# Kernel tuning notes

Measured on AMD Instinct MI355X. Metric: run time of the kernel, lower is better.

## Reference

```python
import jax, jax.numpy as jnp
import numpy as np

VOCAB, EMBED = 100000, 128
B, QLEN, DLEN = 1024, 32, 256
KERNEL_NUM, SIGMA, EXACT_SIGMA = 11, 0.1, 0.001
EPS = 1e-8  # torch F.cosine_similarity eps


def _kernel_mus(n):
    l_mu = [1.0]
    if n == 1:
        return l_mu
    bin_size = 2.0 / (n - 1)
    l_mu.append(1 - bin_size / 2)
    for i in range(1, n - 1):
        l_mu.append(round(l_mu[i] - bin_size, 5))
    return list(reversed(l_mu))


def _kernel_sigmas(n, sigma, exact_sigma):
    l_sigma = [exact_sigma]
    if n == 1:
        return l_sigma
    l_sigma += [sigma] * (n - 1)
    return list(reversed(l_sigma))


MUS = jnp.asarray(np.array(_kernel_mus(KERNEL_NUM), dtype=np.float32))      # [K]
SIGMAS = jnp.asarray(np.array(_kernel_sigmas(KERNEL_NUM, SIGMA, EXACT_SIGMA), dtype=np.float32))  # [K]


def setup_inputs() -> dict:
    key = jax.random.key(0)
    k = jax.random.split(key, 7)
    return {
        "emb": jax.random.normal(k[0], (VOCAB, EMBED), dtype=jnp.float32),
        "mlp_w": jax.random.normal(k[1], (1, KERNEL_NUM), dtype=jnp.float32) * 0.3,
        "mlp_b": jax.random.normal(k[2], (1,), dtype=jnp.float32) * 0.1,
        "query1": jax.random.randint(k[3], (B, QLEN), 0, VOCAB, dtype=jnp.int32).astype(jnp.int64),
        "doc1": jax.random.randint(k[4], (B, DLEN), 0, VOCAB, dtype=jnp.int32).astype(jnp.int64),
        "query2": jax.random.randint(k[5], (B, QLEN), 0, VOCAB, dtype=jnp.int32).astype(jnp.int64),
        "doc2": jax.random.randint(k[6], (B, DLEN), 0, VOCAB, dtype=jnp.int32).astype(jnp.int64),
    }


def _predict(emb, mlp_w, mlp_b, query, doc):
    qe = emb[query]                               # [B,Q,E]
    de = emb[doc]                                 # [B,D,E]
    qn = jnp.linalg.norm(qe, axis=-1)             # [B,Q]
    dn = jnp.linalg.norm(de, axis=-1)             # [B,D]
    dots = jnp.einsum("bqe,bde->bqd", qe, de)    # [B,Q,D]
    sim = dots / jnp.maximum(qn[:, :, None] * dn[:, None, :], EPS)
    # multi-Gaussian soft histogram: exp(-(sim-mu)^2/(2 sigma^2)), sum over doc,
    # log1p, sum over query  -> [B,K]
    z = (sim[..., None] - MUS) / SIGMAS           # [B,Q,D,K]
    K = jnp.exp(-0.5 * z * z)
    pooled = jnp.log1p(K.sum(axis=2)).sum(axis=1)  # [B,K]
    return pooled @ mlp_w.T + mlp_b               # [B,1]


def reference(emb, mlp_w, mlp_b, query1, doc1, query2, doc2):
    logits_1 = _predict(emb, mlp_w, mlp_b, query1, doc1)
    logits_2 = _predict(emb, mlp_w, mlp_b, query2, doc2)
    return jax.nn.sigmoid(logits_1 - logits_2)    # [B,1]
```

## Files before the change

kernel.cpp:

```cpp
#include <hip/hip_runtime.h>
#include <math.h>

#define VOCAB 100000
#define NB    1024
#define QLEN  32
#define DLEN  256
#define EMBED 128
#define KNUM  11

typedef __attribute__((ext_vector_type(8))) short bf16x8;
typedef __attribute__((ext_vector_type(4))) float f32x4;

#define HALF_L2E 0.7213475204444817f
#define TWO_L2E  2.8853900817779268f
#define EM4      0.018315638888734179f

#define SSTR  68
#define SHALF (16 * SSTR)

__global__ __launch_bounds__(256)
void cvt_table(const float* __restrict__ emb, ushort* __restrict__ ebf,
               float* __restrict__ inorm)
{
    const int row = blockIdx.x * 8 + (threadIdx.x >> 5);
    const int l32 = threadIdx.x & 31;
    const float4 v = *((const float4*)(emb + (size_t)row * EMBED) + l32);
    union { float f; unsigned u; } x0, x1, x2, x3;
    x0.f = v.x; x1.f = v.y; x2.f = v.z; x3.f = v.w;
    const unsigned r0 = x0.u + 0x8000u, r1 = x1.u + 0x8000u;
    const unsigned r2 = x2.u + 0x8000u, r3 = x3.u + 0x8000u;
    uint2 packed;
    packed.x = (r0 >> 16) | (r1 & 0xFFFF0000u);
    packed.y = (r2 >> 16) | (r3 & 0xFFFF0000u);
    *((uint2*)(ebf + (size_t)row * EMBED) + l32) = packed;
    x0.u = r0 & 0xFFFF0000u; x1.u = r1 & 0xFFFF0000u;
    x2.u = r2 & 0xFFFF0000u; x3.u = r3 & 0xFFFF0000u;
    float n = x0.f * x0.f + x1.f * x1.f + x2.f * x2.f + x3.f * x3.f;
    #pragma unroll
    for (int m = 1; m < 32; m <<= 1) n += __shfl_xor(n, m);
    if (l32 == 0) inorm[row] = __builtin_amdgcn_rsqf(n);
}

__device__ __forceinline__ bf16x8 cvt8(const float* p, float& nacc)
{
    uint4 a = *((const uint4*)p);
    uint4 b = *((const uint4*)(p + 4));
    unsigned u[8] = {a.x, a.y, a.z, a.w, b.x, b.y, b.z, b.w};
    bf16x8 r;
    #pragma unroll
    for (int i = 0; i < 8; ++i) {
        const unsigned q = u[i] + 0x8000u;
        r[i] = (short)(q >> 16);
        union { unsigned uu; float ff; } g; g.uu = q & 0xFFFF0000u;
        nacc = fmaf(g.ff, g.ff, nacc);
    }
    return r;
}

__device__ __forceinline__ void pool_half(float* __restrict__ wtile,
                                          const f32x4* __restrict__ a,
                                          const float* __restrict__ riq,
                                          const float* __restrict__ idn,
                                          float (*__restrict__ stot)[12],
                                          int mtbase, int l15, int quad)
{
    #pragma unroll
    for (int nt = 0; nt < 4; ++nt)
        #pragma unroll
        for (int r = 0; r < 4; ++r)
            wtile[(quad * 4 + r) * SSTR + nt * 16 + l15] = a[nt][r] * riq[r] * idn[nt];

    const float* rp = wtile + l15 * SSTR + quad * 16;
    float ksum[KNUM];
    #pragma unroll
    for (int k = 0; k < KNUM; ++k) ksum[k] = 0.f;

    #pragma unroll
    for (int i = 0; i < 4; ++i) {
        const f32x4 sv = *((const f32x4*)(rp + 4 * i));
        #pragma unroll
        for (int e = 0; e < 4; ++e) {
            const float s  = sv[e];
            const float z  = fmaf(s, 10.f, -1.f);
            const float e0 = exp2f(-HALF_L2E * (z * z));
            float ru = exp2f(fmaf(z,  TWO_L2E, -TWO_L2E));
            float rd = exp2f(fmaf(z, -TWO_L2E, -TWO_L2E));
            ksum[5] += e0;
            float tt = e0;
            tt *= ru; ksum[6] += tt; ru *= EM4;
            tt *= ru; ksum[7] += tt; ru *= EM4;
            tt *= ru; ksum[8] += tt; ru *= EM4;
            tt *= ru; ksum[9] += tt;
            tt = e0;
            tt *= rd; ksum[4] += tt; rd *= EM4;
            tt *= rd; ksum[3] += tt; rd *= EM4;
            tt *= rd; ksum[2] += tt; rd *= EM4;
            tt *= rd; ksum[1] += tt; rd *= EM4;
            tt *= rd; ksum[0] += tt;
            ksum[10] += (s > 0.995f) ? 1.f : 0.f;
        }
    }
    #pragma unroll
    for (int k = 0; k < KNUM; ++k) {
        ksum[k] += __shfl_xor(ksum[k], 16);
        ksum[k] += __shfl_xor(ksum[k], 32);
    }
    if (quad == 0) {
        #pragma unroll
        for (int k = 0; k < KNUM; ++k)
            atomicAdd(&stot[mtbase + l15][k], ksum[k]);
    }
}

template<bool PRE>
__global__ __launch_bounds__(256, 2)
void knrm_fused(const float* __restrict__ emb,
                const ushort* __restrict__ ebf,
                const float* __restrict__ inorm,
                const float* __restrict__ mlp_w,
                const int* __restrict__ q1, const int* __restrict__ d1,
                const int* __restrict__ q2, const int* __restrict__ d2,
                float* __restrict__ out)
{
    const int b    = blockIdx.x;
    const int t    = threadIdx.x;
    const int w    = t >> 6;
    const int l15  = t & 15;
    const int quad = (t & 63) >> 4;

    const int* __restrict__ qryA = q1 + b * QLEN;
    const int* __restrict__ docA = d1 + b * DLEN;
    const int* __restrict__ qryB = q2 + b * QLEN;
    const int* __restrict__ docB = d2 + b * DLEN;

    __shared__ __align__(16) float s_sim[4 * SHALF];
    __shared__ float s_tot[2][QLEN][12];

    #pragma unroll
    for (int i = t; i < 2 * QLEN * 12; i += 256) ((float*)s_tot)[i] = 0.f;
    __syncthreads();

    const int qidA0 = qryA[l15], qidA1 = qryA[l15 + 16];
    const int qidB0 = qryB[l15], qidB1 = qryB[l15 + 16];
    int didA[4], didB[4];
    #pragma unroll
    for (int nt = 0; nt < 4; ++nt) {
        didA[nt] = docA[(w * 4 + nt) * 16 + l15];
        didB[nt] = docB[(w * 4 + nt) * 16 + l15];
    }

    f32x4 acc[2][4];
    #pragma unroll
    for (int mt = 0; mt < 2; ++mt)
        #pragma unroll
        for (int nt = 0; nt < 4; ++nt)
            acc[mt][nt] = (f32x4){0.f, 0.f, 0.f, 0.f};

    float idnA[4], idnB[4], riqA[2][4], riqB[2][4];
    float* wtile = s_sim + w * SHALF;

    if (PRE) {
        const ushort* qa0 = ebf + (size_t)qidA0 * EMBED + quad * 8;
        const ushort* qa1 = ebf + (size_t)qidA1 * EMBED + quad * 8;
        #pragma unroll
        for (int kk = 0; kk < 4; ++kk) {
            const bf16x8 a0 = *((const bf16x8*)(qa0 + kk * 32));
            const bf16x8 a1 = *((const bf16x8*)(qa1 + kk * 32));
            #pragma unroll
            for (int nt = 0; nt < 4; ++nt) {
                const bf16x8 bb = *((const bf16x8*)(ebf + (size_t)didA[nt] * EMBED + quad * 8 + kk * 32));
                acc[0][nt] = __builtin_amdgcn_mfma_f32_16x16x32_bf16(a0, bb, acc[0][nt], 0, 0, 0);
                acc[1][nt] = __builtin_amdgcn_mfma_f32_16x16x32_bf16(a1, bb, acc[1][nt], 0, 0, 0);
            }
        }

        bf16x8 pq0[4], pq1[4], pdb[4][4];
        const ushort* qb0 = ebf + (size_t)qidB0 * EMBED + quad * 8;
        const ushort* qb1 = ebf + (size_t)qidB1 * EMBED + quad * 8;
        #pragma unroll
        for (int kk = 0; kk < 4; ++kk) {
            pq0[kk] = *((const bf16x8*)(qb0 + kk * 32));
            pq1[kk] = *((const bf16x8*)(qb1 + kk * 32));
            #pragma unroll
            for (int nt = 0; nt < 4; ++nt)
                pdb[nt][kk] = *((const bf16x8*)(ebf + (size_t)didB[nt] * EMBED + quad * 8 + kk * 32));
        }
        #pragma unroll
        for (int nt = 0; nt < 4; ++nt) { idnA[nt] = inorm[didA[nt]]; idnB[nt] = inorm[didB[nt]]; }
        #pragma unroll
        for (int r = 0; r < 4; ++r) {
            riqA[0][r] = inorm[qryA[quad * 4 + r]];
            riqA[1][r] = inorm[qryA[16 + quad * 4 + r]];
            riqB[0][r] = inorm[qryB[quad * 4 + r]];
            riqB[1][r] = inorm[qryB[16 + quad * 4 + r]];
        }

        pool_half(wtile, acc[0], riqA[0], idnA, s_tot[0], 0,  l15, quad);
        pool_half(wtile, acc[1], riqA[1], idnA, s_tot[0], 16, l15, quad);

        #pragma unroll
        for (int mt = 0; mt < 2; ++mt)
            #pragma unroll
            for (int nt = 0; nt < 4; ++nt)
                acc[mt][nt] = (f32x4){0.f, 0.f, 0.f, 0.f};
        #pragma unroll
        for (int kk = 0; kk < 4; ++kk)
            #pragma unroll
            for (int nt = 0; nt < 4; ++nt) {
                acc[0][nt] = __builtin_amdgcn_mfma_f32_16x16x32_bf16(pq0[kk], pdb[nt][kk], acc[0][nt], 0, 0, 0);
                acc[1][nt] = __builtin_amdgcn_mfma_f32_16x16x32_bf16(pq1[kk], pdb[nt][kk], acc[1][nt], 0, 0, 0);
            }

        pool_half(wtile, acc[0], riqB[0], idnB, s_tot[1], 0,  l15, quad);
        pool_half(wtile, acc[1], riqB[1], idnB, s_tot[1], 16, l15, quad);
    } else {
        #pragma unroll
        for (int p = 0; p < 2; ++p) {
            const int* qry = p == 0 ? qryA : qryB;
            const int qi0 = p == 0 ? qidA0 : qidB0;
            const int qi1 = p == 0 ? qidA1 : qidB1;
            const int* did = p == 0 ? didA : didB;
            float qn2[2] = {0.f, 0.f}, dn2[4] = {0.f, 0.f, 0.f, 0.f};
            #pragma unroll
            for (int mt = 0; mt < 2; ++mt)
                #pragma unroll
                for (int nt = 0; nt < 4; ++nt)
                    acc[mt][nt] = (f32x4){0.f, 0.f, 0.f, 0.f};
            const float* qp0 = emb + (size_t)qi0 * EMBED + quad * 8;
            const float* qp1 = emb + (size_t)qi1 * EMBED + quad * 8;
            #pragma unroll
            for (int kk = 0; kk < 4; ++kk) {
                const bf16x8 a0 = cvt8(qp0 + kk * 32, qn2[0]);
                const bf16x8 a1 = cvt8(qp1 + kk * 32, qn2[1]);
                #pragma unroll
                for (int nt = 0; nt < 4; ++nt) {
                    const bf16x8 bb = cvt8(emb + (size_t)did[nt] * EMBED + quad * 8 + kk * 32, dn2[nt]);
                    acc[0][nt] = __builtin_amdgcn_mfma_f32_16x16x32_bf16(a0, bb, acc[0][nt], 0, 0, 0);
                    acc[1][nt] = __builtin_amdgcn_mfma_f32_16x16x32_bf16(a1, bb, acc[1][nt], 0, 0, 0);
                }
            }
            float idn[4], riq[2][4];
            #pragma unroll
            for (int i = 0; i < 2; ++i) {
                qn2[i] += __shfl_xor(qn2[i], 16);
                qn2[i] += __shfl_xor(qn2[i], 32);
            }
            #pragma unroll
            for (int nt = 0; nt < 4; ++nt) {
                dn2[nt] += __shfl_xor(dn2[nt], 16);
                dn2[nt] += __shfl_xor(dn2[nt], 32);
                idn[nt] = __builtin_amdgcn_rsqf(dn2[nt]);
            }
            #pragma unroll
            for (int r = 0; r < 4; ++r) {
                riq[0][r] = __builtin_amdgcn_rsqf(__shfl(qn2[0], quad * 4 + r));
                riq[1][r] = __builtin_amdgcn_rsqf(__shfl(qn2[1], quad * 4 + r));
            }
            pool_half(wtile, acc[0], riq[0], idn, s_tot[p], 0,  l15, quad);
            pool_half(wtile, acc[1], riq[1], idn, s_tot[p], 16, l15, quad);
        }
    }
    __syncthreads();

    if (t < QLEN) {
        float c = 0.f;
        #pragma unroll
        for (int k = 0; k < KNUM; ++k)
            c += mlp_w[k] * (log1pf(s_tot[0][t][k]) - log1pf(s_tot[1][t][k]));
        #pragma unroll
        for (int mm = 1; mm < 32; mm <<= 1) c += __shfl_xor(c, mm);
        if (t == 0) out[b] = 1.f / (1.f + __expf(-c));
    }
}

extern "C" void kernel_launch(void* const* d_in, const int* in_sizes, int n_in,
                              void* d_out, int out_size, void* d_ws, size_t ws_size,
                              hipStream_t stream)
{
    const float* emb   = (const float*)d_in[0];
    const float* mlp_w = (const float*)d_in[1];
    const int* q1 = (const int*)d_in[3];
    const int* d1 = (const int*)d_in[4];
    const int* q2 = (const int*)d_in[5];
    const int* d2 = (const int*)d_in[6];

    float* out = (float*)d_out;

    const size_t need = (size_t)VOCAB * 4
                      + (size_t)VOCAB * EMBED * 2 + 256;
    if (ws_size >= need) {
        float*  inorm = (float*)d_ws;
        ushort* ebf   = (ushort*)(inorm + VOCAB);
        cvt_table<<<VOCAB / 8, 256, 0, stream>>>(emb, ebf, inorm);
        knrm_fused<true><<<NB, 256, 0, stream>>>(emb, ebf, inorm, mlp_w,
                                                 q1, d1, q2, d2, out);
    } else {
        knrm_fused<false><<<NB, 256, 0, stream>>>(emb, nullptr, nullptr, mlp_w,
                                                  q1, d1, q2, d2, out);
    }
}
```

Baseline: 145.8 us.

## Split query/doc pairs across grid and stage bf16 rows via global_load_lds

The fused kernel, which did both prediction pairs per block, is replaced by a 2D grid with one block per (batch, pair). Each block stages the gathered bf16 embedding rows straight into LDS using global_load_lds, then feeds MFMA from LDS. The goal is more parallel blocks and asynchronous direct-to-LDS gathers in place of register-held loads. The cost is a third kernel launch to combine the logits through sigmoid, plus a larger LDS footprint (about 72KB per block) that may limit occupancy.

```diff
diff --git a/kernel.cpp b/kernel.cpp
--- a/kernel.cpp
+++ b/kernel.cpp
@@ -17,6 +17,13 @@
 
 #define SSTR  68
 #define SHALF (16 * SSTR)
+
+typedef const __attribute__((address_space(1))) unsigned int gu32;
+typedef __attribute__((address_space(3))) unsigned int lu32;
+__device__ __forceinline__ void load_lds16(const void* g, void* l)
+{
+    __builtin_amdgcn_global_load_lds((gu32*)g, (lu32*)l, 16, 0, 0);
+}
 
 __global__ __launch_bounds__(256)
 void cvt_table(const float* __restrict__ emb, ushort* __restrict__ ebf,
@@ -112,15 +119,103 @@
     }
 }
 
-template<bool PRE>
+__global__ __launch_bounds__(256)
+void knrm_pair(const ushort* __restrict__ ebf,
+               const float* __restrict__ inorm,
+               const float* __restrict__ mlp_w,
+               const int* __restrict__ q1, const int* __restrict__ d1,
+               const int* __restrict__ q2, const int* __restrict__ d2,
+               float* __restrict__ logits)
+{
+    const int b    = blockIdx.x;
+    const int pair = blockIdx.y;
+    const int t    = threadIdx.x;
+    const int w    = t >> 6;
+    const int lane = t & 63;
+    const int l15  = t & 15;
+    const int quad = lane >> 4;
+
+    const int* __restrict__ qry = (pair == 0 ? q1 : q2) + b * QLEN;
+    const int* __restrict__ doc = (pair == 0 ? d1 : d2) + b * DLEN;
+
+    __shared__ __align__(16) char s_stage[4 * 16 * 1024 + 8 * 1024];
+    __shared__ float s_tot[QLEN][12];
+    char* dstage = s_stage;
+    char* qstage = s_stage + 4 * 16 * 1024;
+
+    #pragma unroll
+    for (int i = t; i < QLEN * 12; i += 256) ((float*)s_tot)[i] = 0.f;
+
+    int did[4];
+    #pragma unroll
+    for (int nt = 0; nt < 4; ++nt) did[nt] = doc[(w * 4 + nt) * 16 + l15];
+
+    #pragma unroll
+    for (int nt = 0; nt < 4; ++nt)
+        #pragma unroll
+        for (int kk = 0; kk < 4; ++kk)
+            load_lds16(ebf + (size_t)did[nt] * EMBED + quad * 8 + kk * 32,
+                       dstage + (w * 16 + nt * 4 + kk) * 1024);
+
+    #pragma unroll
+    for (int ii = 0; ii < 2; ++ii) {
+        const int idx = w * 2 + ii;
+        const int qtile = idx >> 2, kk = idx & 3;
+        load_lds16(ebf + (size_t)qry[qtile * 16 + l15] * EMBED + quad * 8 + kk * 32,
+                   qstage + idx * 1024);
+    }
+
+    float idn[4], riq[2][4];
+    #pragma unroll
+    for (int nt = 0; nt < 4; ++nt) idn[nt] = inorm[did[nt]];
+    #pragma unroll
+    for (int r = 0; r < 4; ++r) {
+        riq[0][r] = inorm[qry[quad * 4 + r]];
+        riq[1][r] = inorm[qry[16 + quad * 4 + r]];
+    }
+
+    __syncthreads();
+
+    f32x4 acc[2][4];
+    #pragma unroll
+    for (int mt = 0; mt < 2; ++mt)
+        #pragma unroll
+        for (int nt = 0; nt < 4; ++nt)
+            acc[mt][nt] = (f32x4){0.f, 0.f, 0.f, 0.f};
+
+    #pragma unroll
+    for (int kk = 0; kk < 4; ++kk) {
+        const bf16x8 a0 = *((const bf16x8*)(qstage + (0 * 4 + kk) * 1024 + lane * 16));
+        const bf16x8 a1 = *((const bf16x8*)(qstage + (1 * 4 + kk) * 1024 + lane * 16));
+        #pragma unroll
+        for (int nt = 0; nt < 4; ++nt) {
+            const bf16x8 bb = *((const bf16x8*)(dstage + (w * 16 + nt * 4 + kk) * 1024 + lane * 16));
+            acc[0][nt] = __builtin_amdgcn_mfma_f32_16x16x32_bf16(a0, bb, acc[0][nt], 0, 0, 0);
+            acc[1][nt] = __builtin_amdgcn_mfma_f32_16x16x32_bf16(a1, bb, acc[1][nt], 0, 0, 0);
+        }
+    }
+
+    float* wtile = (float*)(dstage + w * 16 * 1024);
+    pool_half(wtile, acc[0], riq[0], idn, s_tot, 0,  l15, quad);
+    pool_half(wtile, acc[1], riq[1], idn, s_tot, 16, l15, quad);
+    __syncthreads();
+
+    if (t < QLEN) {
+        float c = 0.f;
+        #pragma unroll
+        for (int k = 0; k < KNUM; ++k) c += mlp_w[k] * log1pf(s_tot[t][k]);
+        #pragma unroll
+        for (int mm = 1; mm < 32; mm <<= 1) c += __shfl_xor(c, mm);
+        if (t == 0) logits[pair * NB + b] = c;
+    }
+}
+
 __global__ __launch_bounds__(256, 2)
-void knrm_fused(const float* __restrict__ emb,
-                const ushort* __restrict__ ebf,
-                const float* __restrict__ inorm,
-                const float* __restrict__ mlp_w,
-                const int* __restrict__ q1, const int* __restrict__ d1,
-                const int* __restrict__ q2, const int* __restrict__ d2,
-                float* __restrict__ out)
+void knrm_fallback(const float* __restrict__ emb,
+                   const float* __restrict__ mlp_w,
+                   const int* __restrict__ q1, const int* __restrict__ d1,
+                   const int* __restrict__ q2, const int* __restrict__ d2,
+                   float* __restrict__ out)
 {
     const int b    = blockIdx.x;
     const int t    = threadIdx.x;
@@ -128,11 +223,6 @@
     const int l15  = t & 15;
     const int quad = (t & 63) >> 4;
 
-    const int* __restrict__ qryA = q1 + b * QLEN;
-    const int* __restrict__ docA = d1 + b * DLEN;
-    const int* __restrict__ qryB = q2 + b * QLEN;
-    const int* __restrict__ docB = d2 + b * DLEN;
-
     __shared__ __align__(16) float s_sim[4 * SHALF];
     __shared__ float s_tot[2][QLEN][12];
 
@@ -140,125 +230,55 @@
     for (int i = t; i < 2 * QLEN * 12; i += 256) ((float*)s_tot)[i] = 0.f;
     __syncthreads();
 
-    const int qidA0 = qryA[l15], qidA1 = qryA[l15 + 16];
-    const int qidB0 = qryB[l15], qidB1 = qryB[l15 + 16];
-    int didA[4], didB[4];
-    #pragma unroll
-    for (int nt = 0; nt < 4; ++nt) {
-        didA[nt] = docA[(w * 4 + nt) * 16 + l15];
-        didB[nt] = docB[(w * 4 + nt) * 16 + l15];
-    }
-
+    float* wtile = s_sim + w * SHALF;
     f32x4 acc[2][4];
-    #pragma unroll
-    for (int mt = 0; mt < 2; ++mt)
-        #pragma unroll
-        for (int nt = 0; nt < 4; ++nt)
-            acc[mt][nt] = (f32x4){0.f, 0.f, 0.f, 0.f};
-
-    float idnA[4], idnB[4], riqA[2][4], riqB[2][4];
-    float* wtile = s_sim + w * SHALF;
-
-    if (PRE) {
-        const ushort* qa0 = ebf + (size_t)qidA0 * EMBED + quad * 8;
-        const ushort* qa1 = ebf + (size_t)qidA1 * EMBED + quad * 8;
-        #pragma unroll
-        for (int kk = 0; kk < 4; ++kk) {
-            const bf16x8 a0 = *((const bf16x8*)(qa0 + kk * 32));
-            const bf16x8 a1 = *((const bf16x8*)(qa1 + kk * 32));
-            #pragma unroll
-            for (int nt = 0; nt < 4; ++nt) {
-                const bf16x8 bb = *((const bf16x8*)(ebf + (size_t)didA[nt] * EMBED + quad * 8 + kk * 32));
-                acc[0][nt] = __builtin_amdgcn_mfma_f32_16x16x32_bf16(a0, bb, acc[0][nt], 0, 0, 0);
-                acc[1][nt] = __builtin_amdgcn_mfma_f32_16x16x32_bf16(a1, bb, acc[1][nt], 0, 0, 0);
-            }
-        }
-
-        bf16x8 pq0[4], pq1[4], pdb[4][4];
-        const ushort* qb0 = ebf + (size_t)qidB0 * EMBED + quad * 8;
-        const ushort* qb1 = ebf + (size_t)qidB1 * EMBED + quad * 8;
-        #pragma unroll
-        for (int kk = 0; kk < 4; ++kk) {
-            pq0[kk] = *((const bf16x8*)(qb0 + kk * 32));
-            pq1[kk] = *((const bf16x8*)(qb1 + kk * 32));
-            #pragma unroll
-            for (int nt = 0; nt < 4; ++nt)
-                pdb[nt][kk] = *((const bf16x8*)(ebf + (size_t)didB[nt] * EMBED + quad * 8 + kk * 32));
-        }
-        #pragma unroll
-        for (int nt = 0; nt < 4; ++nt) { idnA[nt] = inorm[didA[nt]]; idnB[nt] = inorm[didB[nt]]; }
-        #pragma unroll
-        for (int r = 0; r < 4; ++r) {
-            riqA[0][r] = inorm[qryA[quad * 4 + r]];
-            riqA[1][r] = inorm[qryA[16 + quad * 4 + r]];
-            riqB[0][r] = inorm[qryB[quad * 4 + r]];
-            riqB[1][r] = inorm[qryB[16 + quad * 4 + r]];
-        }
-
-        pool_half(wtile, acc[0], riqA[0], idnA, s_tot[0], 0,  l15, quad);
-        pool_half(wtile, acc[1], riqA[1], idnA, s_tot[0], 16, l15, quad);
-
+
+    #pragma unroll
+    for (int p = 0; p < 2; ++p) {
+        const int* qry = (p == 0 ? q1 : q2) + b * QLEN;
+        const int* doc = (p == 0 ? d1 : d2) + b * DLEN;
+        const int qi0 = qry[l15], qi1 = qry[l15 + 16];
+        int did[4];
+        #pragma unroll
+        for (int nt = 0; nt < 4; ++nt) did[nt] = doc[(w * 4 + nt) * 16 + l15];
+        float qn2[2] = {0.f, 0.f}, dn2[4] = {0.f, 0.f, 0.f, 0.f};
         #pragma unroll
         for (int mt = 0; mt < 2; ++mt)
             #pragma unroll
             for (int nt = 0; nt < 4; ++nt)
                 acc[mt][nt] = (f32x4){0.f, 0.f, 0.f, 0.f};
-        #pragma unroll
-        for (int kk = 0; kk < 4; ++kk)
+        const float* qp0 = emb + (size_t)qi0 * EMBED + quad * 8;
+        const float* qp1 = emb + (size_t)qi1 * EMBED + quad * 8;
+        #pragma unroll
+        for (int kk = 0; kk < 4; ++kk) {
+            const bf16x8 a0 = cvt8(qp0 + kk * 32, qn2[0]);
+            const bf16x8 a1 = cvt8(qp1 + kk * 32, qn2[1]);
             #pragma unroll
             for (int nt = 0; nt < 4; ++nt) {
-                acc[0][nt] = __builtin_amdgcn_mfma_f32_16x16x32_bf16(pq0[kk], pdb[nt][kk], acc[0][nt], 0, 0, 0);
-                acc[1][nt] = __builtin_amdgcn_mfma_f32_16x16x32_bf16(pq1[kk], pdb[nt][kk], acc[1][nt], 0, 0, 0);
+                const bf16x8 bb = cvt8(emb + (size_t)did[nt] * EMBED + quad * 8 + kk * 32, dn2[nt]);
+                acc[0][nt] = __builtin_amdgcn_mfma_f32_16x16x32_bf16(a0, bb, acc[0][nt], 0, 0, 0);
+                acc[1][nt] = __builtin_amdgcn_mfma_f32_16x16x32_bf16(a1, bb, acc[1][nt], 0, 0, 0);
             }
-
-        pool_half(wtile, acc[0], riqB[0], idnB, s_tot[1], 0,  l15, quad);
-        pool_half(wtile, acc[1], riqB[1], idnB, s_tot[1], 16, l15, quad);
-    } else {
-        #pragma unroll
-        for (int p = 0; p < 2; ++p) {
-            const int* qry = p == 0 ? qryA : qryB;
-            const int qi0 = p == 0 ? qidA0 : qidB0;
-            const int qi1 = p == 0 ? qidA1 : qidB1;
-            const int* did = p == 0 ? didA : didB;
-            float qn2[2] = {0.f, 0.f}, dn2[4] = {0.f, 0.f, 0.f, 0.f};
-            #pragma unroll
-            for (int mt = 0; mt < 2; ++mt)
-                #pragma unroll
-                for (int nt = 0; nt < 4; ++nt)
-                    acc[mt][nt] = (f32x4){0.f, 0.f, 0.f, 0.f};
-            const float* qp0 = emb + (size_t)qi0 * EMBED + quad * 8;
-            const float* qp1 = emb + (size_t)qi1 * EMBED + quad * 8;
-            #pragma unroll
-            for (int kk = 0; kk < 4; ++kk) {
-                const bf16x8 a0 = cvt8(qp0 + kk * 32, qn2[0]);
-                const bf16x8 a1 = cvt8(qp1 + kk * 32, qn2[1]);
-                #pragma unroll
-                for (int nt = 0; nt < 4; ++nt) {
-                    const bf16x8 bb = cvt8(emb + (size_t)did[nt] * EMBED + quad * 8 + kk * 32, dn2[nt]);
-                    acc[0][nt] = __builtin_amdgcn_mfma_f32_16x16x32_bf16(a0, bb, acc[0][nt], 0, 0, 0);
-                    acc[1][nt] = __builtin_amdgcn_mfma_f32_16x16x32_bf16(a1, bb, acc[1][nt], 0, 0, 0);
-                }
-            }
-            float idn[4], riq[2][4];
-            #pragma unroll
-            for (int i = 0; i < 2; ++i) {
-                qn2[i] += __shfl_xor(qn2[i], 16);
-                qn2[i] += __shfl_xor(qn2[i], 32);
-            }
-            #pragma unroll
-            for (int nt = 0; nt < 4; ++nt) {
-                dn2[nt] += __shfl_xor(dn2[nt], 16);
-                dn2[nt] += __shfl_xor(dn2[nt], 32);
-                idn[nt] = __builtin_amdgcn_rsqf(dn2[nt]);
-            }
-            #pragma unroll
-            for (int r = 0; r < 4; ++r) {
-                riq[0][r] = __builtin_amdgcn_rsqf(__shfl(qn2[0], quad * 4 + r));
-                riq[1][r] = __builtin_amdgcn_rsqf(__shfl(qn2[1], quad * 4 + r));
-            }
-            pool_half(wtile, acc[0], riq[0], idn, s_tot[p], 0,  l15, quad);
-            pool_half(wtile, acc[1], riq[1], idn, s_tot[p], 16, l15, quad);
-        }
+        }
+        float idn[4], riq[2][4];
+        #pragma unroll
+        for (int i = 0; i < 2; ++i) {
+            qn2[i] += __shfl_xor(qn2[i], 16);
+            qn2[i] += __shfl_xor(qn2[i], 32);
+        }
+        #pragma unroll
+        for (int nt = 0; nt < 4; ++nt) {
+            dn2[nt] += __shfl_xor(dn2[nt], 16);
+            dn2[nt] += __shfl_xor(dn2[nt], 32);
+            idn[nt] = __builtin_amdgcn_rsqf(dn2[nt]);
+        }
+        #pragma unroll
+        for (int r = 0; r < 4; ++r) {
+            riq[0][r] = __builtin_amdgcn_rsqf(__shfl(qn2[0], quad * 4 + r));
+            riq[1][r] = __builtin_amdgcn_rsqf(__shfl(qn2[1], quad * 4 + r));
+        }
+        pool_half(wtile, acc[0], riq[0], idn, s_tot[p], 0,  l15, quad);
+        pool_half(wtile, acc[1], riq[1], idn, s_tot[p], 16, l15, quad);
     }
     __syncthreads();
 
@@ -270,6 +290,16 @@
         #pragma unroll
         for (int mm = 1; mm < 32; mm <<= 1) c += __shfl_xor(c, mm);
         if (t == 0) out[b] = 1.f / (1.f + __expf(-c));
+    }
+}
+
+__global__ __launch_bounds__(256)
+void knrm_combine(const float* __restrict__ logits, float* __restrict__ out)
+{
+    const int i = blockIdx.x * blockDim.x + threadIdx.x;
+    if (i < NB) {
+        const float d = logits[i] - logits[NB + i];
+        out[i] = 1.f / (1.f + __expf(-d));
     }
 }
 
@@ -286,16 +316,19 @@
 
     float* out = (float*)d_out;
 
-    const size_t need = (size_t)VOCAB * 4
+    const size_t need = 2 * NB * 4
+                      + (size_t)VOCAB * 4
                       + (size_t)VOCAB * EMBED * 2 + 256;
     if (ws_size >= need) {
-        float*  inorm = (float*)d_ws;
-        ushort* ebf   = (ushort*)(inorm + VOCAB);
+        float*  logits = (float*)d_ws;
+        float*  inorm  = logits + 2 * NB;
+        ushort* ebf    = (ushort*)(inorm + VOCAB);
         cvt_table<<<VOCAB / 8, 256, 0, stream>>>(emb, ebf, inorm);
-        knrm_fused<true><<<NB, 256, 0, stream>>>(emb, ebf, inorm, mlp_w,
-                                                 q1, d1, q2, d2, out);
+        dim3 grid(NB, 2);
+        knrm_pair<<<grid, 256, 0, stream>>>(ebf, inorm, mlp_w,
+                                            q1, d1, q2, d2, logits);
+        knrm_combine<<<(NB + 255) / 256, 256, 0, stream>>>(logits, out);
     } else {
-        knrm_fused<false><<<NB, 256, 0, stream>>>(emb, nullptr, nullptr, mlp_w,
-                                                  q1, d1, q2, d2, out);
-    }
-}
+        knrm_fallback<<<NB, 256, 0, stream>>>(emb, mlp_w, q1, d1, q2, d2, out);
+    }
+}
```

Result: slower. 156.4 us (+7.3%).
